# Performance work log

Measured on AMD Instinct MI355X. Metric: run time of the kernel, lower is better.

The kernel has to match this reference:

```python
import jax, jax.numpy as jnp
import numpy as np

H = 4          # num attention heads
LRELU = 0.2    # DGL GATConv leaky-relu slope
N_GT, N_AG = 100000, 20000
E_GT, E_COMM = 640000, 320000
D_GT, D_AG = 32, 64
VIS, COMM, MSG, OUT = 64, 128, 64, 5
NUM_COMM_STEPS = 2


def _leaky(x):
    return jnp.where(x >= 0, x, LRELU * x)


def gat(feat_src, feat_dst, w_src, w_dst, a_l, a_r, bias, src, dst, n_dst, dh):
    """Bipartite DGL GATConv: residual=Identity (in_dst == H*dh), activation=ReLU."""
    fs = (feat_src @ w_src).reshape(-1, H, dh)   # [Ns,H,dh]
    fd = (feat_dst @ w_dst).reshape(-1, H, dh)   # [Nd,H,dh]
    el = (fs * a_l[None]).sum(-1)                # [Ns,H]
    er = (fd * a_r[None]).sum(-1)                # [Nd,H]
    e = _leaky(el[src] + er[dst])                # [E,H]
    emax = jax.ops.segment_max(e, dst, num_segments=n_dst)
    ex = jnp.exp(e - emax[dst])
    denom = jax.ops.segment_sum(ex, dst, num_segments=n_dst)
    a = ex / denom[dst]                          # edge softmax over in-edges
    rst = jax.ops.segment_sum(fs[src] * a[..., None], dst, num_segments=n_dst)
    rst = rst + feat_dst.reshape(n_dst, H, dh)   # identity residual
    rst = rst + bias.reshape(1, H, dh)
    return jax.nn.relu(rst).reshape(n_dst, H * dh)


def gru(x, h, w_ih, w_hh, b_ih, b_hh):
    gi = x @ w_ih + b_ih
    gh = h @ w_hh + b_hh
    i_r, i_z, i_n = jnp.split(gi, 3, axis=1)
    h_r, h_z, h_n = jnp.split(gh, 3, axis=1)
    r = jax.nn.sigmoid(i_r + h_r)
    zg = jax.nn.sigmoid(i_z + h_z)
    n = jnp.tanh(i_n + r * h_n)
    return (1.0 - zg) * n + zg * h


def setup_inputs() -> dict:
    key = jax.random.key(0)
    ks = jax.random.split(key, 32)
    def w(k, shp):
        return (jax.random.normal(k, shp, dtype=jnp.float32) / np.sqrt(shp[0])).astype(jnp.float32)
    dh1, dh2 = VIS // H, COMM // H
    inp = {
        'feat_gt': jax.random.normal(ks[0], (N_GT, D_GT), dtype=jnp.float32),
        'feat_agent': jax.random.normal(ks[1], (N_AG, D_AG), dtype=jnp.float32),
        'z': jax.random.normal(ks[2], (N_AG, COMM), dtype=jnp.float32),
        'gt_src': jax.random.randint(ks[3], (E_GT,), 0, N_GT, dtype=jnp.int32),
        'gt_dst': jax.random.randint(ks[4], (E_GT,), 0, N_AG, dtype=jnp.int32),
        'comm_src': jax.random.randint(ks[5], (E_COMM,), 0, N_AG, dtype=jnp.int32),
        'comm_dst': jax.random.randint(ks[6], (E_COMM,), 0, N_AG, dtype=jnp.int32),
        # vis1 GATConv (gt->agent), out 64 = 4 heads x 16
        'w1_src': w(ks[7], (D_GT, VIS)), 'w1_dst': w(ks[8], (D_AG, VIS)),
        'a1_l': w(ks[9], (H, dh1)), 'a1_r': w(ks[10], (H, dh1)),
        'b1': jnp.zeros((VIS,), jnp.float32),
        'w2_src': w(ks[11], (D_GT, COMM)), 'w2_dst': w(ks[12], (VIS + D_AG, COMM)),
        'a2_l': w(ks[13], (H, dh2)), 'a2_r': w(ks[14], (H, dh2)),
        'b2': jnp.zeros((COMM,), jnp.float32),
        # comm f_enc: mlp([128,128,64]) with ReLU everywhere
        'enc_w1': w(ks[15], (COMM, 128)), 'enc_b1': jnp.zeros((128,), jnp.float32),
        'enc_w2': w(ks[16], (128, MSG)), 'enc_b2': jnp.zeros((MSG,), jnp.float32),
        # GRUCell(in=COMM+MSG=192, hidden=COMM=128), stored [in, 3*hidden]
        'gru_w_ih': w(ks[17], (COMM + MSG, 3 * COMM)),
        'gru_w_hh': w(ks[18], (COMM, 3 * COMM)),
        'gru_b_ih': jnp.zeros((3 * COMM,), jnp.float32),
        'gru_b_hh': jnp.zeros((3 * COMM,), jnp.float32),
        # f_out
        'out_w': w(ks[19], (COMM, OUT)), 'out_b': jnp.zeros((OUT,), jnp.float32),
    }
    return inp


def _forward(feat_gt, feat_agent, z, gt_src, gt_dst, comm_src, comm_dst,
             w1_src, w1_dst, a1_l, a1_r, b1,
             w2_src, w2_dst, a2_l, a2_r, b2,
             enc_w1, enc_b1, enc_w2, enc_b2,
             gru_w_ih, gru_w_hh, gru_b_ih, gru_b_hh,
             out_w, out_b):
    n_ag = feat_agent.shape[0]
    h_vis1 = gat(feat_gt, feat_agent, w1_src, w1_dst, a1_l, a1_r, b1,
                 gt_src, gt_dst, n_ag, VIS // H)
    dst2 = jnp.concatenate([h_vis1, feat_agent], axis=1)
    h = gat(feat_gt, dst2, w2_src, w2_dst, a2_l, a2_r, b2,
            gt_src, gt_dst, n_ag, COMM // H)
    deg = jax.ops.segment_sum(jnp.ones_like(comm_dst, dtype=jnp.float32),
                              comm_dst, num_segments=n_ag)
    denom = jnp.maximum(deg, 1.0)[:, None]
    zz = z
    for _ in range(NUM_COMM_STEPS):
        m = jax.nn.relu(jax.nn.relu(h @ enc_w1 + enc_b1) @ enc_w2 + enc_b2)  # per-node f_enc
        y = jax.ops.segment_sum(m[comm_src], comm_dst, num_segments=n_ag) / denom  # mailbox mean
        h = gru(jnp.concatenate([h, y], axis=1), zz, gru_w_ih, gru_w_hh, gru_b_ih, gru_b_hh)
        zz = h
    h_out = h @ out_w + out_b
    return h_out, zz


def reference(feat_gt, feat_agent, z, gt_src, gt_dst, comm_src, comm_dst,
              w1_src, w1_dst, a1_l, a1_r, b1,
              w2_src, w2_dst, a2_l, a2_r, b2,
              enc_w1, enc_b1, enc_w2, enc_b2,
              gru_w_ih, gru_w_hh, gru_b_ih, gru_b_hh,
              out_w, out_b):
    return _forward(feat_gt, feat_agent, z, gt_src, gt_dst, comm_src, comm_dst,
                    w1_src, w1_dst, a1_l, a1_r, b1,
                    w2_src, w2_dst, a2_l, a2_r, b2,
                    enc_w1, enc_b1, enc_w2, enc_b2,
                    gru_w_ih, gru_w_hh, gru_b_ih, gru_b_hh,
                    out_w, out_b)
```

## Files before the change

kernel.cpp:

```cpp
#include <hip/hip_runtime.h>
#include <math.h>

#define NHEAD 4
#define LRELU_S 0.2f
constexpr int N_GT = 100000, N_AG = 20000;
constexpr int E_GT = 640000, E_COMM = 320000;
constexpr int OUTD = 5;
constexpr int NBLK_SC = (N_AG + 255) / 256;
constexpr int MB_GT = (N_GT + 63) / 64;
constexpr int FS_TILES = 3 * MB_GT;
constexpr int ETILES  = (N_AG + 31) / 32;
constexpr int GGROUPS = (N_AG + 3) / 4;

constexpr long O_CNTP_GT = 0;
constexpr long O_CNTP_CM = 320000;
constexpr long O_FSB1    = 0;
constexpr long O_FSB2    = 3200000;
constexpr long O_EL1     = 12800000;
constexpr long O_EL2     = 13200000;
constexpr long O_ER1     = 14880000;
constexpr long O_RST2    = 17600000;
constexpr long O_DINV    = 20160000;
constexpr long O_OFFS_GT = 20180000;
constexpr long O_SRT_GT  = 20200004;
constexpr long O_OFFS_CM = 20840004;
constexpr long O_SRT_CM  = 20860008;
constexpr long O_PART    = 21180008;
constexpr long O_V       = 21220008;
constexpr long O_WB      = 21300000;
constexpr long O_RANK_GT = 21500000;
constexpr long O_RANK_CM = 22140000;
constexpr long O_M  = 10240000;
constexpr long O_Y  = 15360000;

constexpr long WB_FS  = 0;
constexpr long WB_E1  = 6144;
constexpr long WB_E2  = 22528;
constexpr long WB_RZ  = 30720;
constexpr long WB_GIN = 112640;
constexpr long WB_GHN = 137216;

using bf8      = __attribute__((ext_vector_type(8))) short;
using f32x4v   = __attribute__((ext_vector_type(4))) float;
using ushort8v = __attribute__((ext_vector_type(8))) unsigned short;

__device__ __forceinline__ unsigned short f2bf(float x) {
    unsigned u = __float_as_uint(x);
    u += 0x7FFFu + ((u >> 16) & 1u);
    return (unsigned short)(u >> 16);
}
__device__ __forceinline__ float bf2f(unsigned short u) {
    return __uint_as_float(((unsigned)u) << 16);
}

__global__ __launch_bounds__(256) void p0_k(
    const float* __restrict__ w1s, const float* __restrict__ w1d,
    const float* __restrict__ a1l, const float* __restrict__ a1r,
    const float* __restrict__ w2s, const float* __restrict__ w2d,
    const float* __restrict__ a2l, const float* __restrict__ a2r,
    const float* __restrict__ e1, const float* __restrict__ e2,
    const float* __restrict__ gih, const float* __restrict__ ghh,
    float* __restrict__ ws)
{
    const int tid = (int)(blockIdx.x * 256 + threadIdx.x);
    const int NT  = (int)(gridDim.x * 256);
    unsigned* wsu = reinterpret_cast<unsigned*>(ws);
    unsigned short* wb = reinterpret_cast<unsigned short*>(ws + O_WB);
    for (int i = tid; i < 640000; i += NT) wsu[O_CNTP_GT + i] = 0u;
    for (int i = tid; i < 153600; i += NT) {
        float val;
        if (i < 2048)        { long l = i;          long n = l / 32,  k = l % 32;  val = w1s[k * 64 + n]; }
        else if (i < 6144)   { long l = i - 2048;   long n = l / 32,  k = l % 32;  val = w2s[k * 128 + n]; }
        else if (i < 22528)  { long l = i - 6144;   long n = l / 128, k = l % 128; val = e1[k * 128 + n]; }
        else if (i < 30720)  { long l = i - 22528;  long n = l / 128, k = l % 128; val = e2[k * 64 + n]; }
        else if (i < 112640) { long l = i - 30720;  long n = l / 320, k = l % 320;
                               val = (k < 192) ? gih[k * 384 + n] : ghh[(k - 192) * 384 + n]; }
        else if (i < 137216) { long l = i - 112640; long n = l / 192, k = l % 192; val = gih[k * 384 + 256 + n]; }
        else                 { long l = i - 137216; long n = l / 128, k = l % 128; val = ghh[k * 384 + 256 + n]; }
        wb[i] = f2bf(val);
    }
    if (tid < 1024) {
        const int i = tid;
        const float *wp, *ap; int dh, local;
        if (i < 128)      { wp = w1s; ap = a1l; dh = 16; local = i; }
        else if (i < 384) { wp = w1d; ap = a1r; dh = 16; local = i - 128; }
        else if (i < 512) { wp = w2s; ap = a2l; dh = 32; local = i - 384; }
        else              { wp = w2d; ap = a2r; dh = 32; local = i - 512; }
        int k = local >> 2, hh = local & 3;
        float s = 0.f;
        for (int j = 0; j < dh; ++j) s += wp[k * (4 * dh) + hh * dh + j] * ap[hh * dh + j];
        ws[O_V + i] = s;
    }
}

__global__ __launch_bounds__(256) void p1_k(
    const int* __restrict__ gt_dst, const int* __restrict__ comm_dst,
    const float* __restrict__ feat_gt, const float* __restrict__ feat_agent,
    float* __restrict__ ws)
{
    const int tid = (int)(blockIdx.x * 256 + threadIdx.x);
    unsigned* wsu = reinterpret_cast<unsigned*>(ws);
    if (tid < E_GT) {
        wsu[O_RANK_GT + tid] = atomicAdd(wsu + O_CNTP_GT + (long)gt_dst[tid] * 16, 1u);
    } else if (tid < E_GT + E_COMM) {
        int j = tid - E_GT;
        wsu[O_RANK_CM + j] = atomicAdd(wsu + O_CNTP_CM + (long)comm_dst[j] * 16, 1u);
    }
    const float* v1  = ws + O_V;
    const float* v2  = ws + O_V + 384;
    const float* vr1 = ws + O_V + 128;
    float* el1 = ws + O_EL1;
    float* el2 = ws + O_EL2;
    float* er1 = ws + O_ER1;
    if (tid < N_GT) {
        const int i = tid;
        float a[8] = {};
        const float* fp = feat_gt + (long)i * 32;
        for (int k = 0; k < 32; ++k) {
            float x = fp[k];
#pragma unroll
            for (int j = 0; j < 4; ++j) a[j] += x * v1[4 * k + j];
#pragma unroll
            for (int j = 0; j < 4; ++j) a[4 + j] += x * v2[4 * k + j];
        }
        *reinterpret_cast<float4*>(el1 + 4l * i) = {a[0], a[1], a[2], a[3]};
        *reinterpret_cast<float4*>(el2 + 4l * i) = {a[4], a[5], a[6], a[7]};
    } else if (tid < N_GT + N_AG) {
        int r = tid - N_GT;
        float a0 = 0, a1 = 0, a2 = 0, a3 = 0;
        const float* fp = feat_agent + (long)r * 64;
        for (int k = 0; k < 64; ++k) {
            float x = fp[k];
            a0 += x * vr1[4 * k];     a1 += x * vr1[4 * k + 1];
            a2 += x * vr1[4 * k + 2]; a3 += x * vr1[4 * k + 3];
        }
        *reinterpret_cast<float4*>(er1 + 4l * r) = {a0, a1, a2, a3};
    }
}

__global__ __launch_bounds__(256) void p2_k(float* __restrict__ ws)
{
    __shared__ unsigned shu[256];
    unsigned* wsu = reinterpret_cast<unsigned*>(ws);
    const int b = (int)blockIdx.x, t = (int)threadIdx.x;
    const int g  = (b >= NBLK_SC) ? 1 : 0;
    const int cb = b - g * NBLK_SC;
    const int i  = cb * 256 + t;
    const unsigned* cnt = wsu + (g ? O_CNTP_CM : O_CNTP_GT);
    unsigned c = (i < N_AG) ? cnt[(long)i * 16] : 0u;
    if (g && i < N_AG) ws[O_DINV + i] = 1.0f / fmaxf((float)c, 1.0f);
    shu[t] = c;
    __syncthreads();
    for (int off = 1; off < 256; off <<= 1) {
        unsigned v = (t >= off) ? shu[t - off] : 0u;
        __syncthreads();
        shu[t] += v;
        __syncthreads();
    }
    unsigned* offs = wsu + (g ? O_OFFS_CM : O_OFFS_GT);
    if (i < N_AG) offs[i] = shu[t] - c;
    if (t == 255) wsu[O_PART + b] = shu[255];
}

__global__ __launch_bounds__(256) void p3_k(float* __restrict__ ws)
{
    __shared__ unsigned shu[128];
    unsigned* wsu = reinterpret_cast<unsigned*>(ws);
    const int b = (int)blockIdx.x, t = (int)threadIdx.x;
    const int g  = (b >= NBLK_SC) ? 1 : 0;
    const int cb = b - g * NBLK_SC;
    if (t < 128) shu[t] = (t < cb) ? wsu[O_PART + g * NBLK_SC + t] : 0u;
    __syncthreads();
    for (int off = 64; off >= 1; off >>= 1) {
        if (t < off) shu[t] += shu[t + off];
        __syncthreads();
    }
    const unsigned pre = shu[0];
    unsigned* offs = wsu + (g ? O_OFFS_CM : O_OFFS_GT);
    const int i = cb * 256 + t;
    if (i < N_AG) offs[i] += pre;
    if (b == NBLK_SC - 1 && t == 0)     wsu[O_OFFS_GT + N_AG] = E_GT;
    if (b == 2 * NBLK_SC - 1 && t == 0) wsu[O_OFFS_CM + N_AG] = E_COMM;
}

__global__ __launch_bounds__(256) void p4_k(
    const int* __restrict__ gt_src, const int* __restrict__ gt_dst,
    const int* __restrict__ comm_src, const int* __restrict__ comm_dst,
    const float* __restrict__ A, float* __restrict__ ws)
{
    unsigned* wsu = reinterpret_cast<unsigned*>(ws);
    const int t = (int)threadIdx.x;
    const int tid = (int)(blockIdx.x * 256 + t);
    if (tid < E_GT) {
        wsu[O_SRT_GT + wsu[O_OFFS_GT + gt_dst[tid]] + wsu[O_RANK_GT + tid]] = (unsigned)gt_src[tid];
    } else if (tid < E_GT + E_COMM) {
        int j = tid - E_GT;
        wsu[O_SRT_CM + wsu[O_OFFS_CM + comm_dst[j]] + wsu[O_RANK_CM + j]] = (unsigned)comm_src[j];
    }

    __shared__ __align__(16) unsigned short As[64][40];
    __shared__ __align__(16) unsigned short Bs[64][40];
    const unsigned short* Btc = reinterpret_cast<unsigned short*>(ws + O_WB) + WB_FS;
    unsigned short* fsb1 = reinterpret_cast<unsigned short*>(ws + O_FSB1);
    unsigned short* fsb2 = reinterpret_cast<unsigned short*>(ws + O_FSB2);
    const int lane = t & 63, wv = t >> 6;
    const int wm = wv & 1, wn = wv >> 1;
    const int quad = lane >> 4, l16 = lane & 15;
    const int rA = t >> 3, cA = (t & 7) * 4;
    const int rB = t >> 2, cB = (t & 3) * 8;
    const int tt = (int)blockIdx.x;
    if (tt >= FS_TILES) return;
    const int n0 = (tt % 3) * 64, m0 = (tt / 3) * 64;
#pragma unroll
    for (int half = 0; half < 2; ++half) {
        const int r = rA + half * 32;
        const int row = m0 + r;
        float4 v = {0.f, 0.f, 0.f, 0.f};
        if (row < N_GT) v = *reinterpret_cast<const float4*>(A + (long)row * 32 + cA);
        ushort4 bb;
        bb.x = f2bf(v.x); bb.y = f2bf(v.y); bb.z = f2bf(v.z); bb.w = f2bf(v.w);
        *reinterpret_cast<ushort4*>(&As[r][cA]) = bb;
    }
    *reinterpret_cast<ushort8v*>(&Bs[rB][cB]) =
        *reinterpret_cast<const ushort8v*>(Btc + (long)(n0 + rB) * 32 + cB);
    __syncthreads();
    f32x4v acc[2][2] = {};
    const bf8 a0 = *reinterpret_cast<const bf8*>(&As[wm * 32 + l16][quad * 8]);
    const bf8 a1 = *reinterpret_cast<const bf8*>(&As[wm * 32 + 16 + l16][quad * 8]);
    const bf8 b0v = *reinterpret_cast<const bf8*>(&Bs[wn * 32 + l16][quad * 8]);
    const bf8 b1v = *reinterpret_cast<const bf8*>(&Bs[wn * 32 + 16 + l16][quad * 8]);
    acc[0][0] = __builtin_amdgcn_mfma_f32_16x16x32_bf16(a0, b0v, acc[0][0], 0, 0, 0);
    acc[0][1] = __builtin_amdgcn_mfma_f32_16x16x32_bf16(a0, b1v, acc[0][1], 0, 0, 0);
    acc[1][0] = __builtin_amdgcn_mfma_f32_16x16x32_bf16(a1, b0v, acc[1][0], 0, 0, 0);
    acc[1][1] = __builtin_amdgcn_mfma_f32_16x16x32_bf16(a1, b1v, acc[1][1], 0, 0, 0);
#pragma unroll
    for (int mt = 0; mt < 2; ++mt)
#pragma unroll
        for (int nt = 0; nt < 2; ++nt)
#pragma unroll
            for (int r = 0; r < 4; ++r) {
                const int row = m0 + wm * 32 + mt * 16 + quad * 4 + r;
                const int col = n0 + wn * 32 + nt * 16 + l16;
                if (row < N_GT) {
                    unsigned short v16 = f2bf(acc[mt][nt][r]);
                    if (col < 64) fsb1[(long)row * 64 + col] = v16;
                    else          fsb2[(long)row * 128 + (col - 64)] = v16;
                }
            }
}

__global__ __launch_bounds__(256) void gat12_k(
    const unsigned* __restrict__ offs, const unsigned* __restrict__ ssrc,
    const float* __restrict__ el1, const float* __restrict__ er1,
    const float* __restrict__ el2,
    const unsigned short* __restrict__ fsb1, const unsigned short* __restrict__ fsb2,
    const float* __restrict__ feat_agent,
    const float* __restrict__ b1, const float* __restrict__ b2,
    const float* __restrict__ vr2, float* __restrict__ out)
{
    const int wid = threadIdx.x >> 6, lane = threadIdx.x & 63;
    const int d = blockIdx.x * 4 + wid;
    if (d >= N_AG) return;
    const int h = lane >> 4, ei = lane & 15;
    const unsigned beg = __builtin_amdgcn_readfirstlane(offs[d]);
    const unsigned end = __builtin_amdgcn_readfirstlane(offs[d + 1]);
    const unsigned smax = (unsigned)N_GT - 1u;

    float s = 0.f, acc0 = 0.f;
    {
        const float er_h = er1[4l * d + h];
        for (unsigned base = beg; base < end; base += 16) {
            const unsigned na = min(16u, end - base);
            unsigned sv = ssrc[base + ((unsigned)ei < na ? (unsigned)ei : 0u)];
            sv = min(sv, smax);
            float p = 0.f;
            if ((unsigned)ei < na) {
                float x = el1[4l * sv + h] + er_h;
                x = (x >= 0.f) ? x : LRELU_S * x;
                p = __expf(x);
            }
            unsigned short fw[16];
#pragma unroll
            for (int j = 0; j < 16; ++j) {
                const unsigned sj = min(ssrc[min(base + (unsigned)j, end - 1u)], smax);
                fw[j] = fsb1[(long)sj * 64 + lane];
            }
#pragma unroll
            for (int j = 0; j < 16; ++j) {
                const float pj = __shfl(p, (h << 4) | j);
                s += pj;
                acc0 += pj * bf2f(fw[j]);
            }
        }
    }
    const float inv1 = (s > 0.f) ? 1.f / s : 0.f;
    const float r1 = feat_agent[(long)d * 64 + lane];
    const float o = fmaxf(acc0 * inv1 + r1 + b1[lane], 0.f);

    float e0 = o * vr2[lane * 4 + 0] + r1 * vr2[(64 + lane) * 4 + 0];
    float e1v = o * vr2[lane * 4 + 1] + r1 * vr2[(64 + lane) * 4 + 1];
    float e2v = o * vr2[lane * 4 + 2] + r1 * vr2[(64 + lane) * 4 + 2];
    float e3v = o * vr2[lane * 4 + 3] + r1 * vr2[(64 + lane) * 4 + 3];
#pragma unroll
    for (int off = 1; off < 64; off <<= 1) {
        e0  += __shfl_xor(e0, off);
        e1v += __shfl_xor(e1v, off);
        e2v += __shfl_xor(e2v, off);
        e3v += __shfl_xor(e3v, off);
    }
    const float er_h2 = (h == 0) ? e0 : (h == 1) ? e1v : (h == 2) ? e2v : e3v;

    const int c0 = lane * 2;
    float s2 = 0.f, A0 = 0.f, A1 = 0.f;
    for (unsigned base = beg; base < end; base += 16) {
        const unsigned na = min(16u, end - base);
        unsigned sv = ssrc[base + ((unsigned)ei < na ? (unsigned)ei : 0u)];
        sv = min(sv, smax);
        float p = 0.f;
        if ((unsigned)ei < na) {
            float x = el2[4l * sv + h] + er_h2;
            x = (x >= 0.f) ? x : LRELU_S * x;
            p = __expf(x);
        }
        unsigned fw[16];
#pragma unroll
        for (int j = 0; j < 16; ++j) {
            const unsigned sj = min(ssrc[min(base + (unsigned)j, end - 1u)], smax);
            fw[j] = *reinterpret_cast<const unsigned*>(fsb2 + (long)sj * 128 + c0);
        }
#pragma unroll
        for (int j = 0; j < 16; ++j) {
            const float pj = __shfl(p, (h << 4) | j);
            s2 += pj;
            A0 += pj * __uint_as_float((fw[j] & 0xFFFFu) << 16);
            A1 += pj * __uint_as_float((fw[j] >> 16) << 16);
        }
    }
    const float inv2 = (s2 > 0.f) ? 1.f / s2 : 0.f;
    const float rox = __shfl(o, c0 & 63);
    const float roy = __shfl(o, (c0 + 1) & 63);
    float2 r;
    if (c0 < 64) { r.x = rox; r.y = roy; }
    else r = *reinterpret_cast<const float2*>(feat_agent + (long)d * 64 + (c0 - 64));
    float2 oo;
    oo.x = fmaxf(A0 * inv2 + r.x + b2[c0], 0.f);
    oo.y = fmaxf(A1 * inv2 + r.y + b2[c0 + 1], 0.f);
    *reinterpret_cast<float2*>(out + (long)d * 128 + c0) = oo;
}

__global__ __launch_bounds__(512) void enc_k(
    const float* __restrict__ h,
    const unsigned short* __restrict__ we1, const unsigned short* __restrict__ we2,
    const float* __restrict__ eb1, const float* __restrict__ eb2,
    unsigned short* __restrict__ mb)
{
    __shared__ __align__(16) unsigned short As[32][136];
    __shared__ __align__(16) unsigned short Ts[32][136];
    const int tid = (int)threadIdx.x;
    const int lane = tid & 63, w = tid >> 6;
    const int quad = lane >> 4, l16 = lane & 15;
    const int m0 = (int)blockIdx.x * 32;
#pragma unroll
    for (int it = 0; it < 2; ++it) {
        int idx = tid + it * 512;
        int row = idx >> 5, cc = (idx & 31) * 4;
        int grow = m0 + row;
        float4 v = {0.f, 0.f, 0.f, 0.f};
        if (grow < N_AG) v = *reinterpret_cast<const float4*>(h + (long)grow * 128 + cc);
        ushort4 b;
        b.x = f2bf(v.x); b.y = f2bf(v.y); b.z = f2bf(v.z); b.w = f2bf(v.w);
        *reinterpret_cast<ushort4*>(&As[row][cc]) = b;
    }
    __syncthreads();
    {
        const int j0 = w * 16;
        const unsigned short* p = we1 + (long)(j0 + l16) * 128 + quad * 8;
        bf8 bw[4];
#pragma unroll
        for (int i = 0; i < 4; ++i) bw[i] = *reinterpret_cast<const bf8*>(p + i * 32);
        f32x4v acc[2] = {};
#pragma unroll
        for (int i = 0; i < 4; ++i) {
            const int k0 = i * 32;
            const bf8 a0 = *reinterpret_cast<const bf8*>(&As[l16][k0 + quad * 8]);
            const bf8 a1 = *reinterpret_cast<const bf8*>(&As[16 + l16][k0 + quad * 8]);
            acc[0] = __builtin_amdgcn_mfma_f32_16x16x32_bf16(a0, bw[i], acc[0], 0, 0, 0);
            acc[1] = __builtin_amdgcn_mfma_f32_16x16x32_bf16(a1, bw[i], acc[1], 0, 0, 0);
        }
        const int j = j0 + l16;
        const float bj = eb1[j];
#pragma unroll
        for (int mt = 0; mt < 2; ++mt)
#pragma unroll
            for (int r = 0; r < 4; ++r)
                Ts[mt * 16 + quad * 4 + r][j] = f2bf(fmaxf(acc[mt][r] + bj, 0.f));
    }
    __syncthreads();
    if (w < 4) {
        const int j0 = w * 16;
        const unsigned short* p = we2 + (long)(j0 + l16) * 128 + quad * 8;
        bf8 bw[4];
#pragma unroll
        for (int i = 0; i < 4; ++i) bw[i] = *reinterpret_cast<const bf8*>(p + i * 32);
        f32x4v acc[2] = {};
#pragma unroll
        for (int i = 0; i < 4; ++i) {
            const int k0 = i * 32;
            const bf8 a0 = *reinterpret_cast<const bf8*>(&Ts[l16][k0 + quad * 8]);
            const bf8 a1 = *reinterpret_cast<const bf8*>(&Ts[16 + l16][k0 + quad * 8]);
            acc[0] = __builtin_amdgcn_mfma_f32_16x16x32_bf16(a0, bw[i], acc[0], 0, 0, 0);
            acc[1] = __builtin_amdgcn_mfma_f32_16x16x32_bf16(a1, bw[i], acc[1], 0, 0, 0);
        }
        const int j = j0 + l16;
        const float bj = eb2[j];
#pragma unroll
        for (int mt = 0; mt < 2; ++mt)
#pragma unroll
            for (int r = 0; r < 4; ++r) {
                const int row = m0 + mt * 16 + quad * 4 + r;
                if (row < N_AG)
                    mb[(long)row * 64 + j] = f2bf(fmaxf(acc[mt][r] + bj, 0.f));
            }
    }
}

__global__ __launch_bounds__(256) void gather_k(
    const unsigned* __restrict__ coffs, const unsigned* __restrict__ cssrc,
    const unsigned short* __restrict__ mb, const float* __restrict__ dinv,
    float* __restrict__ y)
{
    const int tid = (int)threadIdx.x;
    const int lane = tid & 63, w = tid >> 6;
    const int d = (int)blockIdx.x * 4 + w;
    if (d >= N_AG) return;
    const unsigned beg  = __builtin_amdgcn_readfirstlane(coffs[d]);
    const unsigned endo = __builtin_amdgcn_readfirstlane(coffs[d + 1]);
    const unsigned smax = (unsigned)N_AG - 1u;
    float acc = 0.f;
    for (unsigned base = beg; base < endo; base += 32) {
        const unsigned na = min(32u, endo - base);
        unsigned short fw[32];
#pragma unroll
        for (int j = 0; j < 32; ++j) {
            const unsigned sj = min(cssrc[min(base + (unsigned)j, endo - 1u)], smax);
            fw[j] = mb[(long)sj * 64 + lane];
        }
#pragma unroll
        for (int j = 0; j < 32; ++j)
            if ((unsigned)j < na) acc += bf2f(fw[j]);
    }
    y[(long)d * 64 + lane] = acc * dinv[d];
}

__global__ __launch_bounds__(512) void gru_k(
    const float* __restrict__ h_in, const float* __restrict__ y, const float* zz,
    const unsigned short* __restrict__ wrz, const unsigned short* __restrict__ wgin,
    const unsigned short* __restrict__ wghn,
    const float* __restrict__ gbih, const float* __restrict__ gbhh,
    float* hout,
    const float* __restrict__ ow, const float* __restrict__ ob, float* __restrict__ outp)
{
    __shared__ __align__(16) unsigned short As[32][328];
    const int tid = (int)threadIdx.x;
    const int lane = tid & 63, w = tid >> 6;
    const int quad = lane >> 4, l16 = lane & 15;
    const int m0 = (int)blockIdx.x * 32;
#pragma unroll
    for (int it = 0; it < 5; ++it) {
        int idx = tid + it * 512;
        int row = idx / 80, cc = (idx - row * 80) * 4;
        int grow = m0 + row;
        float4 v = {0.f, 0.f, 0.f, 0.f};
        if (grow < N_AG) {
            if (cc < 128)      v = *reinterpret_cast<const float4*>(h_in + (long)grow * 128 + cc);
            else if (cc < 192) v = *reinterpret_cast<const float4*>(y + (long)grow * 64 + (cc - 128));
            else               v = *reinterpret_cast<const float4*>(zz + (long)grow * 128 + (cc - 192));
        }
        ushort4 b;
        b.x = f2bf(v.x); b.y = f2bf(v.y); b.z = f2bf(v.z); b.w = f2bf(v.w);
        *reinterpret_cast<ushort4*>(&As[row][cc]) = b;
    }
    __syncthreads();

    f32x4v aR[2] = {}, aZ[2] = {}, aI[2] = {}, aH[2] = {};
    const int j0 = w * 16;
    const unsigned short* pR = wrz + (long)(j0 + l16) * 320 + quad * 8;
    const unsigned short* pZ = wrz + (long)(128 + j0 + l16) * 320 + quad * 8;
#pragma unroll
    for (int half = 0; half < 2; ++half) {
        bf8 bR[5], bZ[5];
#pragma unroll
        for (int i = 0; i < 5; ++i) {
            const int k0 = half * 160 + i * 32;
            bR[i] = *reinterpret_cast<const bf8*>(pR + k0);
            bZ[i] = *reinterpret_cast<const bf8*>(pZ + k0);
        }
#pragma unroll
        for (int i = 0; i < 5; ++i) {
            const int k0 = half * 160 + i * 32;
            const bf8 a0 = *reinterpret_cast<const bf8*>(&As[l16][k0 + quad * 8]);
            const bf8 a1 = *reinterpret_cast<const bf8*>(&As[16 + l16][k0 + quad * 8]);
            aR[0] = __builtin_amdgcn_mfma_f32_16x16x32_bf16(a0, bR[i], aR[0], 0, 0, 0);
            aR[1] = __builtin_amdgcn_mfma_f32_16x16x32_bf16(a1, bR[i], aR[1], 0, 0, 0);
            aZ[0] = __builtin_amdgcn_mfma_f32_16x16x32_bf16(a0, bZ[i], aZ[0], 0, 0, 0);
            aZ[1] = __builtin_amdgcn_mfma_f32_16x16x32_bf16(a1, bZ[i], aZ[1], 0, 0, 0);
        }
    }
    {
        const unsigned short* pI = wgin + (long)(j0 + l16) * 192 + quad * 8;
        bf8 bI[6];
#pragma unroll
        for (int i = 0; i < 6; ++i) bI[i] = *reinterpret_cast<const bf8*>(pI + i * 32);
#pragma unroll
        for (int i = 0; i < 6; ++i) {
            const int k0 = i * 32;
            const bf8 a0 = *reinterpret_cast<const bf8*>(&As[l16][k0 + quad * 8]);
            const bf8 a1 = *reinterpret_cast<const bf8*>(&As[16 + l16][k0 + quad * 8]);
            aI[0] = __builtin_amdgcn_mfma_f32_16x16x32_bf16(a0, bI[i], aI[0], 0, 0, 0);
            aI[1] = __builtin_amdgcn_mfma_f32_16x16x32_bf16(a1, bI[i], aI[1], 0, 0, 0);
        }
    }
    {
        const unsigned short* pH = wghn + (long)(j0 + l16) * 128 + quad * 8;
        bf8 bH[4];
#pragma unroll
        for (int i = 0; i < 4; ++i) bH[i] = *reinterpret_cast<const bf8*>(pH + i * 32);
#pragma unroll
        for (int i = 0; i < 4; ++i) {
            const int k0 = 192 + i * 32;
            const bf8 a0 = *reinterpret_cast<const bf8*>(&As[l16][k0 + quad * 8]);
            const bf8 a1 = *reinterpret_cast<const bf8*>(&As[16 + l16][k0 + quad * 8]);
            aH[0] = __builtin_amdgcn_mfma_f32_16x16x32_bf16(a0, bH[i], aH[0], 0, 0, 0);
            aH[1] = __builtin_amdgcn_mfma_f32_16x16x32_bf16(a1, bH[i], aH[1], 0, 0, 0);
        }
    }
    const int j = j0 + l16;
    float hv[2][4];
#pragma unroll
    for (int mt = 0; mt < 2; ++mt)
#pragma unroll
        for (int r = 0; r < 4; ++r) {
            const int row = m0 + mt * 16 + quad * 4 + r;
            float v = 0.f;
            if (row < N_AG) {
                const float rr = 1.f / (1.f + __expf(-(aR[mt][r] + gbih[j] + gbhh[j])));
                const float zg = 1.f / (1.f + __expf(-(aZ[mt][r] + gbih[128 + j] + gbhh[128 + j])));
                const float nn = tanhf(aI[mt][r] + gbih[256 + j] + rr * (aH[mt][r] + gbhh[256 + j]));
                const float hp = zz[(long)row * 128 + j];
                v = (1.f - zg) * nn + zg * hp;
            }
            hv[mt][r] = v;
        }

    if (outp == nullptr) {
#pragma unroll
        for (int mt = 0; mt < 2; ++mt)
#pragma unroll
            for (int r = 0; r < 4; ++r) {
                const int row = m0 + mt * 16 + quad * 4 + r;
                if (row < N_AG) hout[(long)row * 128 + j] = hv[mt][r];
            }
    } else {
        __syncthreads();
        float* Hs = reinterpret_cast<float*>(&As[0][0]);
#pragma unroll
        for (int mt = 0; mt < 2; ++mt)
#pragma unroll
            for (int r = 0; r < 4; ++r)
                Hs[(mt * 16 + quad * 4 + r) * 128 + j] = hv[mt][r];
        __syncthreads();
        for (int it = tid; it < 32 * 32; it += 512) {
            const int row = it >> 5, c4 = (it & 31) * 4;
            const float4 v = *reinterpret_cast<const float4*>(&Hs[row * 128 + c4]);
            *reinterpret_cast<float4*>(outp + (long)N_AG * OUTD + (long)(m0 + row) * 128 + c4) = v;
        }
        for (int it = tid; it < 32 * OUTD; it += 512) {
            const int row = it / OUTD, jj = it - row * OUTD;
            float a = ob[jj];
            const float* hr = &Hs[row * 128];
            for (int k = 0; k < 128; ++k) a += hr[k] * ow[k * OUTD + jj];
            outp[(long)(m0 + row) * OUTD + jj] = a;
        }
    }
}

extern "C" void kernel_launch(void* const* d_in, const int* in_sizes, int n_in,
                              void* d_out, int out_size, void* d_ws, size_t ws_size,
                              hipStream_t stream) {
    const float* feat_gt    = (const float*)d_in[0];
    const float* feat_agent = (const float*)d_in[1];
    const float* z_in       = (const float*)d_in[2];
    const int*   gt_src     = (const int*)d_in[3];
    const int*   gt_dst     = (const int*)d_in[4];
    const int*   comm_src   = (const int*)d_in[5];
    const int*   comm_dst   = (const int*)d_in[6];
    const float* w1_src = (const float*)d_in[7];
    const float* w1_dst = (const float*)d_in[8];
    const float* a1_l   = (const float*)d_in[9];
    const float* a1_r   = (const float*)d_in[10];
    const float* b1     = (const float*)d_in[11];
    const float* w2_src = (const float*)d_in[12];
    const float* w2_dst = (const float*)d_in[13];
    const float* a2_l   = (const float*)d_in[14];
    const float* a2_r   = (const float*)d_in[15];
    const float* b2     = (const float*)d_in[16];
    const float* enc_w1 = (const float*)d_in[17];
    const float* enc_b1 = (const float*)d_in[18];
    const float* enc_w2 = (const float*)d_in[19];
    const float* enc_b2 = (const float*)d_in[20];
    const float* gw_ih  = (const float*)d_in[21];
    const float* gw_hh  = (const float*)d_in[22];
    const float* gb_ih  = (const float*)d_in[23];
    const float* gb_hh  = (const float*)d_in[24];
    const float* out_w  = (const float*)d_in[25];
    const float* out_b  = (const float*)d_in[26];

    float* ws = (float*)d_ws;
    unsigned* wsu = (unsigned*)d_ws;
    unsigned short* wb = (unsigned short*)(ws + O_WB);
    float* out = (float*)d_out;

    float* hptr = ws + O_RST2;
    unsigned short* mb = (unsigned short*)(ws + O_M);
    float* yb = ws + O_Y;

    p0_k<<<dim3(2500), dim3(256), 0, stream>>>(w1_src, w1_dst, a1_l, a1_r,
                                               w2_src, w2_dst, a2_l, a2_r,
                                               enc_w1, enc_w2, gw_ih, gw_hh, ws);
    p1_k<<<dim3(3750), dim3(256), 0, stream>>>(gt_dst, comm_dst, feat_gt, feat_agent, ws);
    p2_k<<<dim3(2 * NBLK_SC), dim3(256), 0, stream>>>(ws);
    p3_k<<<dim3(2 * NBLK_SC), dim3(256), 0, stream>>>(ws);
    p4_k<<<dim3(FS_TILES), dim3(256), 0, stream>>>(gt_src, gt_dst, comm_src, comm_dst,
                                                   feat_gt, ws);

    gat12_k<<<dim3(GGROUPS), dim3(256), 0, stream>>>(
        wsu + O_OFFS_GT, wsu + O_SRT_GT,
        ws + O_EL1, ws + O_ER1, ws + O_EL2,
        (const unsigned short*)(ws + O_FSB1), (const unsigned short*)(ws + O_FSB2),
        feat_agent, b1, b2, ws + O_V + 512, hptr);

    for (int step = 0; step < 2; ++step) {
        const float* zz = (step == 0) ? z_in : hptr;
        enc_k<<<dim3(ETILES), dim3(512), 0, stream>>>(hptr, wb + WB_E1, wb + WB_E2,
                                                      enc_b1, enc_b2, mb);
        gather_k<<<dim3(GGROUPS), dim3(256), 0, stream>>>(wsu + O_OFFS_CM, wsu + O_SRT_CM,
                                                          mb, ws + O_DINV, yb);
        gru_k<<<dim3(ETILES), dim3(512), 0, stream>>>(hptr, yb, zz, wb + WB_RZ, wb + WB_GIN,
                                                      wb + WB_GHN, gb_ih, gb_hh, hptr,
                                                      (step == 1) ? out_w : nullptr,
                                                      (step == 1) ? out_b : nullptr,
                                                      (step == 1) ? out : nullptr);
    }
}
```

Before: 364.6 us.

## Split GAT edge loops across two waves per node and fuse comm gather into GRU

The GAT kernel now assigns two wavefronts per destination node, each handling half the 16-edge chunks, then combines partial softmax sums and accumulators through shared memory with block barriers. This gives more memory-level parallelism on the gather-bound edge loops. Separately, the mailbox mean gather is folded into the GRU kernel, writing y into shared memory instead of a global buffer, which removes a launch and a global round trip. The risks are extra barriers, doubled per-node work setup, and the GRU blocks doing serial gather work before their MFMA phase.

```diff
diff --git a/kernel.cpp b/kernel.cpp
--- a/kernel.cpp
+++ b/kernel.cpp
@@ -10,7 +10,6 @@
 constexpr int MB_GT = (N_GT + 63) / 64;
 constexpr int FS_TILES = 3 * MB_GT;
 constexpr int ETILES  = (N_AG + 31) / 32;
-constexpr int GGROUPS = (N_AG + 3) / 4;
 
 constexpr long O_CNTP_GT = 0;
 constexpr long O_CNTP_CM = 320000;
@@ -31,7 +30,6 @@
 constexpr long O_RANK_GT = 21500000;
 constexpr long O_RANK_CM = 22140000;
 constexpr long O_M  = 10240000;
-constexpr long O_Y  = 15360000;
 
 constexpr long WB_FS  = 0;
 constexpr long WB_E1  = 6144;
@@ -258,18 +256,28 @@
     const float* __restrict__ b1, const float* __restrict__ b2,
     const float* __restrict__ vr2, float* __restrict__ out)
 {
-    const int wid = threadIdx.x >> 6, lane = threadIdx.x & 63;
-    const int d = blockIdx.x * 4 + wid;
-    if (d >= N_AG) return;
+    __shared__ float cS1[2][2][4];
+    __shared__ float cA1[2][2][64];
+    __shared__ float cS2s[2][2][4];
+    __shared__ float cAB[2][2][2][64];
+    const int tid = (int)threadIdx.x;
+    const int wid = tid >> 6, lane = tid & 63;
+    const int dl = wid >> 1, half = wid & 1;
+    const int d = (int)blockIdx.x * 2 + dl;
     const int h = lane >> 4, ei = lane & 15;
     const unsigned beg = __builtin_amdgcn_readfirstlane(offs[d]);
     const unsigned end = __builtin_amdgcn_readfirstlane(offs[d + 1]);
     const unsigned smax = (unsigned)N_GT - 1u;
+    const unsigned nc  = (end - beg + 15u) >> 4;
+    const unsigned ncA = (nc + 1u) >> 1;
+    const unsigned cb = half ? ncA : 0u;
+    const unsigned ce = half ? nc : ncA;
 
     float s = 0.f, acc0 = 0.f;
     {
         const float er_h = er1[4l * d + h];
-        for (unsigned base = beg; base < end; base += 16) {
+        for (unsigned c = cb; c < ce; ++c) {
+            const unsigned base = beg + c * 16u;
             const unsigned na = min(16u, end - base);
             unsigned sv = ssrc[base + ((unsigned)ei < na ? (unsigned)ei : 0u)];
             sv = min(sv, smax);
@@ -293,9 +301,14 @@
             }
         }
     }
-    const float inv1 = (s > 0.f) ? 1.f / s : 0.f;
+    if (ei == 0) cS1[dl][half][h] = s;
+    cA1[dl][half][lane] = acc0;
+    __syncthreads();
+    const float sT = cS1[dl][0][h] + cS1[dl][1][h];
+    const float aT = cA1[dl][0][lane] + cA1[dl][1][lane];
+    const float inv1 = (sT > 0.f) ? 1.f / sT : 0.f;
     const float r1 = feat_agent[(long)d * 64 + lane];
-    const float o = fmaxf(acc0 * inv1 + r1 + b1[lane], 0.f);
+    const float o = fmaxf(aT * inv1 + r1 + b1[lane], 0.f);
 
     float e0 = o * vr2[lane * 4 + 0] + r1 * vr2[(64 + lane) * 4 + 0];
     float e1v = o * vr2[lane * 4 + 1] + r1 * vr2[(64 + lane) * 4 + 1];
@@ -310,9 +323,10 @@
     }
     const float er_h2 = (h == 0) ? e0 : (h == 1) ? e1v : (h == 2) ? e2v : e3v;
 
-    const int c0 = lane * 2;
+    const int col0 = lane * 2;
     float s2 = 0.f, A0 = 0.f, A1 = 0.f;
-    for (unsigned base = beg; base < end; base += 16) {
+    for (unsigned c = cb; c < ce; ++c) {
+        const unsigned base = beg + c * 16u;
         const unsigned na = min(16u, end - base);
         unsigned sv = ssrc[base + ((unsigned)ei < na ? (unsigned)ei : 0u)];
         sv = min(sv, smax);
@@ -326,7 +340,7 @@
 #pragma unroll
         for (int j = 0; j < 16; ++j) {
             const unsigned sj = min(ssrc[min(base + (unsigned)j, end - 1u)], smax);
-            fw[j] = *reinterpret_cast<const unsigned*>(fsb2 + (long)sj * 128 + c0);
+            fw[j] = *reinterpret_cast<const unsigned*>(fsb2 + (long)sj * 128 + col0);
         }
 #pragma unroll
         for (int j = 0; j < 16; ++j) {
@@ -336,16 +350,25 @@
             A1 += pj * __uint_as_float((fw[j] >> 16) << 16);
         }
     }
-    const float inv2 = (s2 > 0.f) ? 1.f / s2 : 0.f;
-    const float rox = __shfl(o, c0 & 63);
-    const float roy = __shfl(o, (c0 + 1) & 63);
-    float2 r;
-    if (c0 < 64) { r.x = rox; r.y = roy; }
-    else r = *reinterpret_cast<const float2*>(feat_agent + (long)d * 64 + (c0 - 64));
-    float2 oo;
-    oo.x = fmaxf(A0 * inv2 + r.x + b2[c0], 0.f);
-    oo.y = fmaxf(A1 * inv2 + r.y + b2[c0 + 1], 0.f);
-    *reinterpret_cast<float2*>(out + (long)d * 128 + c0) = oo;
+    if (ei == 0) cS2s[dl][half][h] = s2;
+    cAB[dl][half][0][lane] = A0;
+    cAB[dl][half][1][lane] = A1;
+    __syncthreads();
+    if (half == 0) {
+        const float s2T = cS2s[dl][0][h] + cS2s[dl][1][h];
+        const float A0T = cAB[dl][0][0][lane] + cAB[dl][1][0][lane];
+        const float A1T = cAB[dl][0][1][lane] + cAB[dl][1][1][lane];
+        const float inv2 = (s2T > 0.f) ? 1.f / s2T : 0.f;
+        const float rox = __shfl(o, col0 & 63);
+        const float roy = __shfl(o, (col0 + 1) & 63);
+        float2 r;
+        if (col0 < 64) { r.x = rox; r.y = roy; }
+        else r = *reinterpret_cast<const float2*>(feat_agent + (long)d * 64 + (col0 - 64));
+        float2 oo;
+        oo.x = fmaxf(A0T * inv2 + r.x + b2[col0], 0.f);
+        oo.y = fmaxf(A1T * inv2 + r.y + b2[col0 + 1], 0.f);
+        *reinterpret_cast<float2*>(out + (long)d * 128 + col0) = oo;
+    }
 }
 
 __global__ __launch_bounds__(512) void enc_k(
@@ -424,36 +447,11 @@
     }
 }
 
-__global__ __launch_bounds__(256) void gather_k(
+__global__ __launch_bounds__(512) void gru_k(
+    const float* __restrict__ h_in,
     const unsigned* __restrict__ coffs, const unsigned* __restrict__ cssrc,
-    const unsigned short* __restrict__ mb, const float* __restrict__ dinv,
-    float* __restrict__ y)
-{
-    const int tid = (int)threadIdx.x;
-    const int lane = tid & 63, w = tid >> 6;
-    const int d = (int)blockIdx.x * 4 + w;
-    if (d >= N_AG) return;
-    const unsigned beg  = __builtin_amdgcn_readfirstlane(coffs[d]);
-    const unsigned endo = __builtin_amdgcn_readfirstlane(coffs[d + 1]);
-    const unsigned smax = (unsigned)N_AG - 1u;
-    float acc = 0.f;
-    for (unsigned base = beg; base < endo; base += 32) {
-        const unsigned na = min(32u, endo - base);
-        unsigned short fw[32];
-#pragma unroll
-        for (int j = 0; j < 32; ++j) {
-            const unsigned sj = min(cssrc[min(base + (unsigned)j, endo - 1u)], smax);
-            fw[j] = mb[(long)sj * 64 + lane];
-        }
-#pragma unroll
-        for (int j = 0; j < 32; ++j)
-            if ((unsigned)j < na) acc += bf2f(fw[j]);
-    }
-    y[(long)d * 64 + lane] = acc * dinv[d];
-}
-
-__global__ __launch_bounds__(512) void gru_k(
-    const float* __restrict__ h_in, const float* __restrict__ y, const float* zz,
+    const unsigned short* __restrict__ mbx, const float* __restrict__ dinv,
+    const float* zz,
     const unsigned short* __restrict__ wrz, const unsigned short* __restrict__ wgin,
     const unsigned short* __restrict__ wghn,
     const float* __restrict__ gbih, const float* __restrict__ gbhh,
@@ -461,10 +459,37 @@
     const float* __restrict__ ow, const float* __restrict__ ob, float* __restrict__ outp)
 {
     __shared__ __align__(16) unsigned short As[32][328];
+    __shared__ __align__(16) float Ys[32][64];
     const int tid = (int)threadIdx.x;
     const int lane = tid & 63, w = tid >> 6;
     const int quad = lane >> 4, l16 = lane & 15;
     const int m0 = (int)blockIdx.x * 32;
+
+    {
+        const unsigned smax = (unsigned)N_AG - 1u;
+#pragma unroll 1
+        for (int q = 0; q < 4; ++q) {
+            const int d = m0 + w * 4 + q;
+            const unsigned beg  = __builtin_amdgcn_readfirstlane(coffs[d]);
+            const unsigned endo = __builtin_amdgcn_readfirstlane(coffs[d + 1]);
+            float acc = 0.f;
+            for (unsigned base = beg; base < endo; base += 32) {
+                const unsigned na = min(32u, endo - base);
+                unsigned short fw[32];
+#pragma unroll
+                for (int j = 0; j < 32; ++j) {
+                    const unsigned sj = min(cssrc[min(base + (unsigned)j, endo - 1u)], smax);
+                    fw[j] = mbx[(long)sj * 64 + lane];
+                }
+#pragma unroll
+                for (int j = 0; j < 32; ++j)
+                    if ((unsigned)j < na) acc += bf2f(fw[j]);
+            }
+            Ys[w * 4 + q][lane] = acc * dinv[d];
+        }
+    }
+    __syncthreads();
+
 #pragma unroll
     for (int it = 0; it < 5; ++it) {
         int idx = tid + it * 512;
@@ -473,7 +498,7 @@
         float4 v = {0.f, 0.f, 0.f, 0.f};
         if (grow < N_AG) {
             if (cc < 128)      v = *reinterpret_cast<const float4*>(h_in + (long)grow * 128 + cc);
-            else if (cc < 192) v = *reinterpret_cast<const float4*>(y + (long)grow * 64 + (cc - 128));
+            else if (cc < 192) v = *reinterpret_cast<const float4*>(&Ys[row][cc - 128]);
             else               v = *reinterpret_cast<const float4*>(zz + (long)grow * 128 + (cc - 192));
         }
         ushort4 b;
@@ -622,7 +647,6 @@
 
     float* hptr = ws + O_RST2;
     unsigned short* mb = (unsigned short*)(ws + O_M);
-    float* yb = ws + O_Y;
 
     p0_k<<<dim3(2500), dim3(256), 0, stream>>>(w1_src, w1_dst, a1_l, a1_r,
                                                w2_src, w2_dst, a2_l, a2_r,
@@ -633,7 +657,7 @@
     p4_k<<<dim3(FS_TILES), dim3(256), 0, stream>>>(gt_src, gt_dst, comm_src, comm_dst,
                                                    feat_gt, ws);
 
-    gat12_k<<<dim3(GGROUPS), dim3(256), 0, stream>>>(
+    gat12_k<<<dim3(N_AG / 2), dim3(256), 0, stream>>>(
         wsu + O_OFFS_GT, wsu + O_SRT_GT,
         ws + O_EL1, ws + O_ER1, ws + O_EL2,
         (const unsigned short*)(ws + O_FSB1), (const unsigned short*)(ws + O_FSB2),
@@ -643,10 +667,11 @@
         const float* zz = (step == 0) ? z_in : hptr;
         enc_k<<<dim3(ETILES), dim3(512), 0, stream>>>(hptr, wb + WB_E1, wb + WB_E2,
                                                       enc_b1, enc_b2, mb);
-        gather_k<<<dim3(GGROUPS), dim3(256), 0, stream>>>(wsu + O_OFFS_CM, wsu + O_SRT_CM,
-                                                          mb, ws + O_DINV, yb);
-        gru_k<<<dim3(ETILES), dim3(512), 0, stream>>>(hptr, yb, zz, wb + WB_RZ, wb + WB_GIN,
-                                                      wb + WB_GHN, gb_ih, gb_hh, hptr,
+        gru_k<<<dim3(ETILES), dim3(512), 0, stream>>>(hptr,
+                                                      wsu + O_OFFS_CM, wsu + O_SRT_CM,
+                                                      mb, ws + O_DINV, zz,
+                                                      wb + WB_RZ, wb + WB_GIN, wb + WB_GHN,
+                                                      gb_ih, gb_hh, hptr,
                                                       (step == 1) ? out_w : nullptr,
                                                       (step == 1) ? out_b : nullptr,
                                                       (step == 1) ? out : nullptr);
```

Result: slower. 441.5 us (+21.1%).
